# Performance work log

Hardware: AMD Instinct MI355X
Metric: run time of the kernel (lower is better)

The kernel has to match this reference:

```python
import jax, jax.numpy as jnp
import numpy as np

N_UP, N_DOWN = 8, 8
N_ELEC = N_UP + N_DOWN
N_NUC = 4
D, K, F, H = 128, 64, 32, 45  # embedding, kernel, dist_feat, w-MLP hidden (log-spaced)
CUTOFF = 10.0
B = 2048


def _pairs(a, b):
    s, r = np.meshgrid(a, b, indexing='ij')
    return s.ravel(), r.ravel()


def _edges():
    up = np.arange(N_UP)
    dn = np.arange(N_UP, N_ELEC)
    su, ru = _pairs(up, up); m = su != ru; su, ru = su[m], ru[m]
    sd, rd = _pairs(dn, dn); m = sd != rd; sd, rd = sd[m], rd[m]
    same_s = np.concatenate([su, sd]); same_r = np.concatenate([ru, rd])
    a1s, a1r = _pairs(up, dn); a2s, a2r = _pairs(dn, up)
    anti_s = np.concatenate([a1s, a2s]); anti_r = np.concatenate([a1r, a2r])
    ne_s = np.repeat(np.arange(N_NUC), N_ELEC)
    ne_r = np.tile(np.arange(N_ELEC), N_NUC)
    return tuple(jnp.asarray(x, jnp.int32) for x in (same_s, same_r, anti_s, anti_r, ne_s, ne_r))


def setup_inputs() -> dict:
    key = jax.random.key(0)
    ks = jax.random.split(key, 10)
    rs = jax.random.normal(ks[0], (B, N_ELEC, 3)) * 2.0
    coords = jax.random.normal(ks[1], (N_NUC, 3)) * 2.0
    X_tab = jax.random.normal(ks[2], (1, D))
    Y_w = jax.random.normal(ks[3], (N_NUC, K)) / np.sqrt(N_NUC)
    wW1 = jax.random.normal(ks[4], (3, 3, F, H)) / np.sqrt(F)
    wb1 = jax.random.normal(ks[5], (3, 3, H)) * 0.1
    wW2 = jax.random.normal(ks[6], (3, 3, H, K)) / np.sqrt(H)
    h0_tab = jax.random.normal(ks[7], (2, 1, K))
    hW = jax.random.normal(ks[8], (2, 2, D, K)) / np.sqrt(D)
    gW = jax.random.normal(ks[9], (3, 3, K, D)) / np.sqrt(K)
    same_s, same_r, anti_s, anti_r, ne_s, ne_r = _edges()
    return dict(rs=rs, coords=coords, X_tab=X_tab, Y_w=Y_w, wW1=wW1, wb1=wb1,
                wW2=wW2, h0_tab=h0_tab, hW=hW, gW=gW,
                same_s=same_s, same_r=same_r, anti_s=anti_s, anti_r=anti_r,
                ne_s=ne_s, ne_r=ne_r)


def _dist_basis(d):
    # DistanceBasis with 'nocusp' envelope: env = d^2 exp(-d), gaussians at mus
    qs = jnp.linspace(0.0, 1.0, F)
    mus = CUTOFF * qs ** 2
    sigmas = (1.0 + CUTOFF * qs) / 7.0
    env = d ** 2 * jnp.exp(-d)
    return env[..., None] * jnp.exp(-((d[..., None] - mus) ** 2) / sigmas ** 2)


def reference(rs, coords, X_tab, Y_w, wW1, wb1, wW2, h0_tab, hW, gW,
              same_s, same_r, anti_s, anti_r, ne_s, ne_r):
    Bn = rs.shape[0]
    spin_idxs = jnp.zeros((N_ELEC,), jnp.int32)  # n_up == n_down -> one spin class
    # per-edge distances (layer-0 update_edges_fn featurizes them once)
    d_same = jnp.linalg.norm(rs[:, same_s] - rs[:, same_r], axis=-1)  # [B,112]
    d_anti = jnp.linalg.norm(rs[:, anti_s] - rs[:, anti_r], axis=-1)  # [B,128]
    d_ne = jnp.linalg.norm(coords[ne_s][None] - rs[:, ne_r], axis=-1)  # [B,64]
    feats = [_dist_basis(d_same), _dist_basis(d_anti), _dist_basis(d_ne)]
    senders = [same_s, anti_s, ne_s]
    receivers = [same_r, anti_r, ne_r]
    elec = X_tab[spin_idxs]  # [N_ELEC, D] electron embedding X(spin_idxs)
    nuc = Y_w                # Y(eye(n_nuc)) == Y_w, [N_NUC, K]
    for l in range(3):
        upd = 0.0
        for j in range(3):  # same, anti, ne
            # w subnet: 2-layer MLP, silu hidden with bias, bias-free linear out
            we = jax.nn.silu(feats[j] @ wW1[l, j] + wb1[l, j]) @ wW2[l, j]  # [B,E,K]
            if j < 2:
                if l == 0:
                    hx = h0_tab[j][spin_idxs][senders[j]]            # [E,K] embed
                else:
                    hx = (elec @ hW[l - 1, j])[:, senders[j]]        # [B,E,K]
                weh = we * hx
            else:
                weh = we * nuc[ne_s][None]                           # [B,E,K]
            # segment_sum scatter into receiver electrons
            z = jnp.zeros((Bn, N_ELEC, K), we.dtype).at[:, receivers[j]].add(weh)
            upd = upd + z @ gW[l, j]                                  # [B,N_ELEC,D]
        elec = elec + upd
    return elec
```

## Files before the change

kernel.cpp:

```cpp
#include <hip/hip_runtime.h>
#include <hip/hip_bf16.h>

#define NE 16
#define NN 4
#define DDIM 128
#define KD 64
#define HD 45

typedef _Float16 half8 __attribute__((ext_vector_type(8)));
typedef _Float16 half4 __attribute__((ext_vector_type(4)));
typedef float floatx4 __attribute__((ext_vector_type(4)));

#define OFF_FLAG_B 0
#define OFF_B1_B   64
#define OFF_XT_B   1792
#define OFF_H0_B   2304
#define OFF_YW_B   2560
#define OFF_W1_B   3072
#define OFF_W2_B   30720
#define OFF_GW_B   104448
#define OFF_HW_B   251904
#define OFF_IND_B  317440

__device__ __forceinline__ float ldf(const void* p, long i, int f32) {
    if (f32) return ((const float*)p)[i];
    unsigned int u = ((unsigned int)((const unsigned short*)p)[i]) << 16;
    return __uint_as_float(u);
}

__global__ void prep2_kernel(const void* w1, const void* b1, const void* w2, const void* h0,
                             const void* hW, const void* gW, const void* Yw, const void* Xt,
                             const void* rs,
                             const int* __restrict__ same_r, const int* __restrict__ anti_r,
                             const int* __restrict__ ne_r, char* wsB) {
    __shared__ int badS;
    if (threadIdx.x == 0) badS = 0;
    __syncthreads();
    {
        const unsigned short* rs16 = (const unsigned short*)rs;
        int bad = 0;
        for (int i = threadIdx.x; i < 2048; i += 256) {
            unsigned int u = ((unsigned int)rs16[i]) << 16;
            float v = __uint_as_float(u);
            if (!(fabsf(v) < 1e6f)) bad = 1;
        }
        if (bad) atomicOr(&badS, 1);
    }
    __syncthreads();
    const int f32 = badS ? 1 : 0;
    if (blockIdx.x == 0 && threadIdx.x == 0) *(int*)(wsB + OFF_FLAG_B) = f32;

    int i = blockIdx.x * 256 + threadIdx.x;
    _Float16* W1F = (_Float16*)(wsB + OFF_W1_B);
    _Float16* W2F = (_Float16*)(wsB + OFF_W2_B);
    _Float16* GWF = (_Float16*)(wsB + OFF_GW_B);
    _Float16* HWF = (_Float16*)(wsB + OFF_HW_B);
    _Float16* INDF= (_Float16*)(wsB + OFF_IND_B);
    float*    B1  = (float*)(wsB + OFF_B1_B);
    float*    XT  = (float*)(wsB + OFF_XT_B);
    _Float16* H0F = (_Float16*)(wsB + OFF_H0_B);
    _Float16* YWF = (_Float16*)(wsB + OFF_YW_B);

    if (i < 13824) {
        int lj = i / 1536, rem = i % 1536;
        int nt = rem >> 9, lane = (rem & 511) >> 3, e = rem & 7;
        int row = ((lane >> 4) << 3) + e;
        int col = (nt << 4) + (lane & 15);
        W1F[i] = (_Float16)((col < 45) ? ldf(w1, lj * 1440 + row * 45 + col, f32) : 0.f);
    }
    if (i < 36864) {
        int lj = i / 4096, rem = i & 4095;
        int nt = rem >> 10, kt = (rem >> 9) & 1, lane = (rem & 511) >> 3, e = rem & 7;
        int row = (kt << 5) + ((lane >> 4) << 3) + e;
        int col = (nt << 4) + (lane & 15);
        W2F[i] = (_Float16)((row < 45) ? ldf(w2, lj * 2880 + row * 64 + col, f32) : 0.f);
    }
    if (i < 73728) {
        int lj = i >> 13, rem = i & 8191;
        int nt = rem >> 10, kt = (rem >> 9) & 1, lane = (rem & 511) >> 3, e = rem & 7;
        int row = (kt << 5) + ((lane >> 4) << 3) + e;
        int col = (nt << 4) + (lane & 15);
        GWF[i] = (_Float16)ldf(gW, lj * 8192 + row * 128 + col, f32);
    }
    if (i < 32768) {
        int lj = i >> 13, rem = i & 8191;
        int nt = rem >> 11, kt = (rem >> 9) & 3, lane = (rem & 511) >> 3, e = rem & 7;
        int row = (kt << 5) + ((lane >> 4) << 3) + e;
        int col = (nt << 4) + (lane & 15);
        HWF[i] = (_Float16)ldf(hW, lj * 8192 + row * 64 + col, f32);
    }
    if (i < 5120) {
        int c = i >> 9, rem = i & 511;
        int ln = rem >> 3, ii = rem & 7;
        int cls = (c < 4) ? 0 : ((c < 8) ? 1 : 2);
        int lc  = c - ((cls == 0) ? 0 : ((cls == 1) ? 4 : 8));
        int qd = ln >> 4, lm = ln & 15;
        int e = lc * 32 + qd * 8 + ii;
        int cnt = (cls == 0) ? 112 : ((cls == 1) ? 128 : 64);
        int r = 255;
        if (e < cnt) r = (cls == 0) ? same_r[e] : ((cls == 1) ? anti_r[e] : ne_r[e]);
        INDF[i] = (r == lm) ? (_Float16)1.0f : (_Float16)0.0f;
    }
    if (i < 432) { int lj = i / 48, n = i % 48; B1[i] = (n < 45) ? ldf(b1, lj * 45 + n, f32) : 0.f; }
    if (i < 128) XT[i] = ldf(Xt, i, f32);
    if (i < 128) H0F[i] = (_Float16)ldf(h0, i, f32);
    if (i < 256) YWF[i] = (_Float16)ldf(Yw, i, f32);
}

__device__ __forceinline__ half8 feat_tile(
    const void* __restrict__ rs, const void* __restrict__ coords,
    int b, int lm, int f32, int tloc, int cls,
    const int* __restrict__ S, const int* __restrict__ R,
    const float* __restrict__ A0, const float* __restrict__ B0, const float* __restrict__ C0)
{
    int le = tloc * 16 + lm;
    int s = S[le], r = R[le];
    long rb = ((long)b * NE + r) * 3;
    float bx = ldf(rs, rb + 0, f32), by = ldf(rs, rb + 1, f32), bz = ldf(rs, rb + 2, f32);
    float ax, ay, az;
    if (cls < 2) {
        long sb = ((long)b * NE + s) * 3;
        ax = ldf(rs, sb + 0, f32); ay = ldf(rs, sb + 1, f32); az = ldf(rs, sb + 2, f32);
    } else {
        ax = ldf(coords, s * 3 + 0, f32); ay = ldf(coords, s * 3 + 1, f32); az = ldf(coords, s * 3 + 2, f32);
    }
    float dx = ax - bx, dy = ay - by, dz = az - bz;
    float d = sqrtf(dx * dx + dy * dy + dz * dz);
    float d2 = d * d;
    half8 a;
    #pragma unroll
    for (int ii = 0; ii < 8; ++ii) {
        float E = fmaf(A0[ii], d2, fmaf(B0[ii], d, C0[ii]));
        a[ii] = (_Float16)(d2 * __expf(E));
    }
    return a;
}

__device__ __forceinline__ void we_tile_weh(
    half8 fa, int lj, int tile,
    const char* __restrict__ wsB, _Float16* __restrict__ hid,
    const _Float16* __restrict__ hxrow,
    const unsigned char* __restrict__ sendC,
    _Float16* __restrict__ wehT,
    int lane, int qd, int lm)
{
    const half8* W1F_lj = (const half8*)(wsB + OFF_W1_B) + lj * 192;
    half8 w0 = W1F_lj[lane], w1v = W1F_lj[64 + lane], w2v = W1F_lj[128 + lane];
    const float* B1 = (const float*)(wsB + OFF_B1_B) + lj * 48;
    float bi0 = B1[lm], bi1 = B1[16 + lm], bi2 = B1[32 + lm];
    floatx4 c0 = {0.f,0.f,0.f,0.f}, c1 = c0, c2 = c0;
    c0 = __builtin_amdgcn_mfma_f32_16x16x32_f16(fa, w0,  c0, 0, 0, 0);
    c1 = __builtin_amdgcn_mfma_f32_16x16x32_f16(fa, w1v, c1, 0, 0, 0);
    c2 = __builtin_amdgcn_mfma_f32_16x16x32_f16(fa, w2v, c2, 0, 0, 0);
    #pragma unroll
    for (int rr = 0; rr < 4; ++rr) {
        int row = qd * 4 + rr;
        int x = (row & 7) << 4;
        float v0 = c0[rr] + bi0, v1 = c1[rr] + bi1, v2 = c2[rr] + bi2;
        v0 = v0 * __builtin_amdgcn_rcpf(1.f + __expf(-v0));
        v1 = v1 * __builtin_amdgcn_rcpf(1.f + __expf(-v1));
        v2 = v2 * __builtin_amdgcn_rcpf(1.f + __expf(-v2));
        char* hb = (char*)hid + row * 128;
        *(_Float16*)(hb + ((lm * 2)      ^ x)) = (_Float16)v0;
        *(_Float16*)(hb + ((32 + lm * 2) ^ x)) = (_Float16)v1;
        *(_Float16*)(hb + ((64 + lm * 2) ^ x)) = (_Float16)v2;
    }
    int xr = (lm & 7) << 4;
    half8 a0 = *(const half8*)((const char*)hid + lm * 128 + ((qd * 16)      ^ xr));
    half8 a1 = *(const half8*)((const char*)hid + lm * 128 + ((64 + qd * 16) ^ xr));

    int sv0 = sendC[tile * 16 + qd * 4 + 0];
    int sv1 = sendC[tile * 16 + qd * 4 + 1];
    int sv2 = sendC[tile * 16 + qd * 4 + 2];
    int sv3 = sendC[tile * 16 + qd * 4 + 3];

    const half8* W2F_lj = (const half8*)(wsB + OFF_W2_B) + lj * 512;
    #pragma unroll
    for (int nt = 0; nt < 4; ++nt) {
        half8 bk0 = W2F_lj[nt * 128 + lane], bk1 = W2F_lj[nt * 128 + 64 + lane];
        floatx4 acc = {0.f,0.f,0.f,0.f};
        acc = __builtin_amdgcn_mfma_f32_16x16x32_f16(a0, bk0, acc, 0, 0, 0);
        acc = __builtin_amdgcn_mfma_f32_16x16x32_f16(a1, bk1, acc, 0, 0, 0);
        const int kc = nt * 16 + lm;
        const int eb = tile * 16 + qd * 4;
        wehT[kc * 136 + eb + 0] = (_Float16)(acc[0] * (float)hxrow[sv0 * 68 + kc]);
        wehT[kc * 136 + eb + 1] = (_Float16)(acc[1] * (float)hxrow[sv1 * 68 + kc]);
        wehT[kc * 136 + eb + 2] = (_Float16)(acc[2] * (float)hxrow[sv2 * 68 + kc]);
        wehT[kc * 136 + eb + 3] = (_Float16)(acc[3] * (float)hxrow[sv3 * 68 + kc]);
    }
}

__device__ __forceinline__ void z_mfma4(
    const _Float16* __restrict__ wehT, const half8* __restrict__ INDF, int c0,
    _Float16* __restrict__ zh, int wv, int qd, int lm, int lane)
{
    const _Float16* base = wehT + (wv * 16 + lm) * 136 + qd * 8;
    floatx4 zD = {0.f,0.f,0.f,0.f};
    zD = __builtin_amdgcn_mfma_f32_16x16x32_f16(*(const half8*)(base +  0), INDF[(c0 + 0) * 64 + lane], zD, 0, 0, 0);
    zD = __builtin_amdgcn_mfma_f32_16x16x32_f16(*(const half8*)(base + 32), INDF[(c0 + 1) * 64 + lane], zD, 0, 0, 0);
    zD = __builtin_amdgcn_mfma_f32_16x16x32_f16(*(const half8*)(base + 64), INDF[(c0 + 2) * 64 + lane], zD, 0, 0, 0);
    zD = __builtin_amdgcn_mfma_f32_16x16x32_f16(*(const half8*)(base + 96), INDF[(c0 + 3) * 64 + lane], zD, 0, 0, 0);
    half4 h;
    #pragma unroll
    for (int i = 0; i < 4; ++i) h[i] = (_Float16)zD[i];
    *(half4*)(zh + lm * 72 + wv * 16 + qd * 4) = h;
}

__device__ __forceinline__ void z_mfma2(
    const _Float16* __restrict__ wehT, const half8* __restrict__ INDF, int c0,
    _Float16* __restrict__ zh, int wv, int qd, int lm, int lane)
{
    const _Float16* base = wehT + (wv * 16 + lm) * 136 + qd * 8;
    floatx4 zD = {0.f,0.f,0.f,0.f};
    zD = __builtin_amdgcn_mfma_f32_16x16x32_f16(*(const half8*)(base +  0), INDF[(c0 + 0) * 64 + lane], zD, 0, 0, 0);
    zD = __builtin_amdgcn_mfma_f32_16x16x32_f16(*(const half8*)(base + 32), INDF[(c0 + 1) * 64 + lane], zD, 0, 0, 0);
    half4 h;
    #pragma unroll
    for (int i = 0; i < 4; ++i) h[i] = (_Float16)zD[i];
    *(half4*)(zh + lm * 72 + wv * 16 + qd * 4) = h;
}

__device__ __forceinline__ void gw_accum(
    int L, int j, int wv, int lane, int qd, int lm,
    const _Float16* __restrict__ zh, const half8* __restrict__ GWF, floatx4 (&eacc)[2])
{
    half8 zf0 = *(const half8*)(zh + lm * 72 + qd * 8);
    half8 zf1 = *(const half8*)(zh + lm * 72 + 32 + qd * 8);
    const half8* G = GWF + (size_t)(L * 3 + j) * 1024;
    #pragma unroll
    for (int u = 0; u < 2; ++u) {
        int t2 = wv * 2 + u;
        eacc[u] = __builtin_amdgcn_mfma_f32_16x16x32_f16(zf0, G[t2 * 128 + lane],      eacc[u], 0, 0, 0);
        eacc[u] = __builtin_amdgcn_mfma_f32_16x16x32_f16(zf1, G[t2 * 128 + 64 + lane], eacc[u], 0, 0, 0);
    }
}

__global__ __launch_bounds__(256, 2)
void fused_kernel(const void* __restrict__ rs, const void* __restrict__ coords,
                  const int* __restrict__ same_s, const int* __restrict__ same_r,
                  const int* __restrict__ anti_s, const int* __restrict__ anti_r,
                  const int* __restrict__ ne_s,   const int* __restrict__ ne_r,
                  const char* __restrict__ wsB, void* __restrict__ out)
{
    const int b = blockIdx.x;
    const int tid = threadIdx.x;
    const int wv = tid >> 6, lane = tid & 63;
    const int qd = lane >> 4, lm = lane & 15;
    const int f32 = *(const int*)(wsB + OFF_FLAG_B);

    __shared__ __align__(16) _Float16 wehT[64 * 136];
    __shared__ __align__(16) _Float16 hidA[4][1024];
    __shared__ __align__(16) _Float16 zhS[16 * 72];
    __shared__ _Float16 hxS[2 * 1088];
    __shared__ _Float16 nucS[4 * 68];
    __shared__ __align__(16) _Float16 elecB[16 * 136];
    __shared__ unsigned char sendPad[384];

    const _Float16* H0F = (const _Float16*)(wsB + OFF_H0_B);
    const _Float16* YWF = (const _Float16*)(wsB + OFF_YW_B);
    const float*    XT  = (const float*)(wsB + OFF_XT_B);
    const half8*    GWF = (const half8*)(wsB + OFF_GW_B);
    const half8*    HWF = (const half8*)(wsB + OFF_HW_B);
    const half8*    INDF= (const half8*)(wsB + OFF_IND_B);

    for (int i = tid; i < 384; i += 256) {
        int cls = i >> 7, pos = i & 127;
        int cnt = (cls == 0) ? 112 : ((cls == 1) ? 128 : 64);
        int s = 0;
        if (pos < cnt) {
            if (cls == 0)      s = same_s[pos];
            else if (cls == 1) s = anti_s[pos];
            else               s = ne_s[pos];
        }
        sendPad[i] = (unsigned char)s;
    }
    for (int i = tid; i < 2048; i += 256)
        hxS[(i >> 10) * 1088 + ((i >> 6) & 15) * 68 + (i & 63)] = H0F[((i >> 10) << 6) + (i & 63)];
    if (tid < 256) nucS[(tid >> 6) * 68 + (tid & 63)] = YWF[tid];
    for (int i = tid; i < 4352; i += 256) ((unsigned int*)wehT)[i] = 0u;
    {
        _Float16* hid = hidA[wv];
        half8 z8 = {0,0,0,0,0,0,0,0};
        *(half8*)(hid + lane * 8) = z8;
        *(half8*)(hid + 512 + lane * 8) = z8;
    }
    __syncthreads();

    half8 fa_s0, fa_s1 = {0,0,0,0,0,0,0,0}, fa_a0, fa_a1, fa_n;
    {
        float A0[8], B0[8], C0[8];
        #pragma unroll
        for (int ii = 0; ii < 8; ++ii) {
            float qf = (float)(qd * 8 + ii) * (1.f / 31.f);
            float mu = 10.f * qf * qf;
            float u = 7.f * __builtin_amdgcn_rcpf(1.f + 10.f * qf);
            float is2 = u * u;
            A0[ii] = -is2;
            B0[ii] = 2.f * mu * is2 - 1.f;
            C0[ii] = -(mu * mu) * is2;
        }
        fa_s0 = feat_tile(rs, coords, b, lm, f32, wv,     0, same_s, same_r, A0, B0, C0);
        if (wv < 3)
        fa_s1 = feat_tile(rs, coords, b, lm, f32, wv + 4, 0, same_s, same_r, A0, B0, C0);
        fa_a0 = feat_tile(rs, coords, b, lm, f32, wv,     1, anti_s, anti_r, A0, B0, C0);
        fa_a1 = feat_tile(rs, coords, b, lm, f32, wv + 4, 1, anti_s, anti_r, A0, B0, C0);
        fa_n  = feat_tile(rs, coords, b, lm, f32, wv,     2, ne_s,   ne_r,   A0, B0, C0);
    }

    floatx4 eacc[2];
    #pragma unroll
    for (int u = 0; u < 2; ++u) {
        float xv = XT[(wv * 2 + u) * 16 + lm];
        eacc[u][0] = xv; eacc[u][1] = xv; eacc[u][2] = xv; eacc[u][3] = xv;
    }

    _Float16* hid = hidA[wv];

    for (int L = 0; L < 3; ++L) {
        const int lj0 = L * 3;
        we_tile_weh(fa_s0, lj0, wv, wsB, hid, hxS, sendPad, wehT, lane, qd, lm);
        if (wv < 3)
        we_tile_weh(fa_s1, lj0, wv + 4, wsB, hid, hxS, sendPad, wehT, lane, qd, lm);
        __syncthreads();
        z_mfma4(wehT, INDF, 0, zhS, wv, qd, lm, lane);
        __syncthreads();
        gw_accum(L, 0, wv, lane, qd, lm, zhS, GWF, eacc);
        we_tile_weh(fa_a0, lj0 + 1, wv,     wsB, hid, hxS + 1088, sendPad + 128, wehT, lane, qd, lm);
        we_tile_weh(fa_a1, lj0 + 1, wv + 4, wsB, hid, hxS + 1088, sendPad + 128, wehT, lane, qd, lm);
        __syncthreads();
        z_mfma4(wehT, INDF, 4, zhS, wv, qd, lm, lane);
        __syncthreads();
        gw_accum(L, 1, wv, lane, qd, lm, zhS, GWF, eacc);
        we_tile_weh(fa_n, lj0 + 2, wv, wsB, hid, nucS, sendPad + 256, wehT, lane, qd, lm);
        __syncthreads();
        z_mfma2(wehT, INDF, 8, zhS, wv, qd, lm, lane);
        __syncthreads();
        gw_accum(L, 2, wv, lane, qd, lm, zhS, GWF, eacc);

        if (L < 2) {
            #pragma unroll
            for (int u = 0; u < 2; ++u) {
                int t2 = wv * 2 + u;
                #pragma unroll
                for (int r = 0; r < 4; ++r)
                    elecB[(qd * 4 + r) * 136 + t2 * 16 + lm] = (_Float16)eacc[u][r];
            }
            __syncthreads();
            half8 ae[4];
            #pragma unroll
            for (int kt = 0; kt < 4; ++kt)
                ae[kt] = *(const half8*)(elecB + lm * 136 + kt * 32 + qd * 8);
            #pragma unroll
            for (int u = 0; u < 2; ++u) {
                int idx = wv * 2 + u;
                int j = idx >> 2, nt = idx & 3;
                floatx4 acc = {0.f,0.f,0.f,0.f};
                #pragma unroll
                for (int kt = 0; kt < 4; ++kt) {
                    half8 g = HWF[(size_t)(((L * 2 + j) * 4 + nt) * 4 + kt) * 64 + lane];
                    acc = __builtin_amdgcn_mfma_f32_16x16x32_f16(ae[kt], g, acc, 0, 0, 0);
                }
                #pragma unroll
                for (int r = 0; r < 4; ++r)
                    hxS[j * 1088 + (qd * 4 + r) * 68 + nt * 16 + lm] = (_Float16)acc[r];
            }
            __syncthreads();
        }
    }

    if (f32) {
        float* o = (float*)out + (size_t)b * 2048;
        #pragma unroll
        for (int u = 0; u < 2; ++u)
            #pragma unroll
            for (int r = 0; r < 4; ++r)
                o[(qd * 4 + r) * 128 + (wv * 2 + u) * 16 + lm] = eacc[u][r];
    } else {
        __hip_bfloat16* o = (__hip_bfloat16*)out + (size_t)b * 2048;
        #pragma unroll
        for (int u = 0; u < 2; ++u)
            #pragma unroll
            for (int r = 0; r < 4; ++r)
                o[(qd * 4 + r) * 128 + (wv * 2 + u) * 16 + lm] = __float2bfloat16(eacc[u][r]);
    }
}

extern "C" void kernel_launch(void* const* d_in, const int* in_sizes, int n_in,
                              void* d_out, int out_size, void* d_ws, size_t ws_size,
                              hipStream_t stream) {
    const void* rs     = d_in[0];
    const void* coords = d_in[1];
    const void* X_tab  = d_in[2];
    const void* Y_w    = d_in[3];
    const void* wW1    = d_in[4];
    const void* wb1    = d_in[5];
    const void* wW2    = d_in[6];
    const void* h0     = d_in[7];
    const void* hW     = d_in[8];
    const void* gW     = d_in[9];
    const int* same_s = (const int*)d_in[10];
    const int* same_r = (const int*)d_in[11];
    const int* anti_s = (const int*)d_in[12];
    const int* anti_r = (const int*)d_in[13];
    const int* ne_s   = (const int*)d_in[14];
    const int* ne_r   = (const int*)d_in[15];
    char* wsB = (char*)d_ws;

    const int Bn = in_sizes[0] / (NE * 3);

    prep2_kernel<<<288, 256, 0, stream>>>(wW1, wb1, wW2, h0, hW, gW, Y_w, X_tab, rs,
                                          same_r, anti_r, ne_r, wsB);
    fused_kernel<<<Bn, 256, 0, stream>>>(rs, coords, same_s, same_r, anti_s, anti_r,
                                         ne_s, ne_r, wsB, d_out);
}
```

Baseline: 187.0 us.

## Process two batch samples per block to amortize barriers and weight loads

Each workgroup now handles two batch elements, duplicating the LDS scratch buffers and interleaving both samples' stages between the same barriers. Each barrier and each block's setup now covers twice the work, and the two independent chains give the scheduler more instructions to overlap. The per-block weh writes also become packed half4 stores instead of scalar stores. In exchange, LDS use roughly doubles and register pressure rises, which can lower occupancy, and the grid is halved to 1024 blocks.

```diff
diff --git a/kernel.cpp b/kernel.cpp
--- a/kernel.cpp
+++ b/kernel.cpp
@@ -183,10 +183,12 @@
         acc = __builtin_amdgcn_mfma_f32_16x16x32_f16(a1, bk1, acc, 0, 0, 0);
         const int kc = nt * 16 + lm;
         const int eb = tile * 16 + qd * 4;
-        wehT[kc * 136 + eb + 0] = (_Float16)(acc[0] * (float)hxrow[sv0 * 68 + kc]);
-        wehT[kc * 136 + eb + 1] = (_Float16)(acc[1] * (float)hxrow[sv1 * 68 + kc]);
-        wehT[kc * 136 + eb + 2] = (_Float16)(acc[2] * (float)hxrow[sv2 * 68 + kc]);
-        wehT[kc * 136 + eb + 3] = (_Float16)(acc[3] * (float)hxrow[sv3 * 68 + kc]);
+        half4 hv;
+        hv[0] = (_Float16)(acc[0] * (float)hxrow[sv0 * 68 + kc]);
+        hv[1] = (_Float16)(acc[1] * (float)hxrow[sv1 * 68 + kc]);
+        hv[2] = (_Float16)(acc[2] * (float)hxrow[sv2 * 68 + kc]);
+        hv[3] = (_Float16)(acc[3] * (float)hxrow[sv3 * 68 + kc]);
+        *(half4*)(wehT + kc * 136 + eb) = hv;
     }
 }
 
@@ -235,25 +237,52 @@
     }
 }
 
+__device__ __forceinline__ void hx_update(
+    int L, int wv, int lane, int qd, int lm,
+    const _Float16* __restrict__ elecB, const half8* __restrict__ HWF,
+    _Float16* __restrict__ hxS)
+{
+    half8 ae0 = *(const half8*)(elecB + lm * 136 +  0 + qd * 8);
+    half8 ae1 = *(const half8*)(elecB + lm * 136 + 32 + qd * 8);
+    half8 ae2 = *(const half8*)(elecB + lm * 136 + 64 + qd * 8);
+    half8 ae3 = *(const half8*)(elecB + lm * 136 + 96 + qd * 8);
+    #pragma unroll
+    for (int u = 0; u < 2; ++u) {
+        int idx = wv * 2 + u;
+        int j = idx >> 2, nt = idx & 3;
+        const half8* Bb = HWF + (size_t)(((L * 2 + j) * 4 + nt) * 4) * 64;
+        floatx4 acc = {0.f,0.f,0.f,0.f};
+        acc = __builtin_amdgcn_mfma_f32_16x16x32_f16(ae0, Bb[  0 + lane], acc, 0, 0, 0);
+        acc = __builtin_amdgcn_mfma_f32_16x16x32_f16(ae1, Bb[ 64 + lane], acc, 0, 0, 0);
+        acc = __builtin_amdgcn_mfma_f32_16x16x32_f16(ae2, Bb[128 + lane], acc, 0, 0, 0);
+        acc = __builtin_amdgcn_mfma_f32_16x16x32_f16(ae3, Bb[192 + lane], acc, 0, 0, 0);
+        #pragma unroll
+        for (int r = 0; r < 4; ++r)
+            hxS[j * 1088 + (qd * 4 + r) * 68 + nt * 16 + lm] = (_Float16)acc[r];
+    }
+}
+
 __global__ __launch_bounds__(256, 2)
 void fused_kernel(const void* __restrict__ rs, const void* __restrict__ coords,
                   const int* __restrict__ same_s, const int* __restrict__ same_r,
                   const int* __restrict__ anti_s, const int* __restrict__ anti_r,
                   const int* __restrict__ ne_s,   const int* __restrict__ ne_r,
-                  const char* __restrict__ wsB, void* __restrict__ out)
-{
-    const int b = blockIdx.x;
+                  const char* __restrict__ wsB, void* __restrict__ out, int Bn)
+{
+    const int b0 = blockIdx.x * 2;
+    const int b1 = b0 + 1;
+    const bool has1 = (b1 < Bn);
     const int tid = threadIdx.x;
     const int wv = tid >> 6, lane = tid & 63;
     const int qd = lane >> 4, lm = lane & 15;
     const int f32 = *(const int*)(wsB + OFF_FLAG_B);
 
-    __shared__ __align__(16) _Float16 wehT[64 * 136];
-    __shared__ __align__(16) _Float16 hidA[4][1024];
-    __shared__ __align__(16) _Float16 zhS[16 * 72];
-    __shared__ _Float16 hxS[2 * 1088];
+    __shared__ __align__(16) _Float16 wehT0[64 * 136], wehT1[64 * 136];
+    __shared__ __align__(16) _Float16 hid0A[4][1024], hid1A[4][1024];
+    __shared__ __align__(16) _Float16 zh0S[16 * 72], zh1S[16 * 72];
+    __shared__ _Float16 hx0S[2 * 1088], hx1S[2 * 1088];
     __shared__ _Float16 nucS[4 * 68];
-    __shared__ __align__(16) _Float16 elecB[16 * 136];
+    __shared__ __align__(16) _Float16 elec0B[16 * 136], elec1B[16 * 136];
     __shared__ unsigned char sendPad[384];
 
     const _Float16* H0F = (const _Float16*)(wsB + OFF_H0_B);
@@ -274,19 +303,27 @@
         }
         sendPad[i] = (unsigned char)s;
     }
-    for (int i = tid; i < 2048; i += 256)
-        hxS[(i >> 10) * 1088 + ((i >> 6) & 15) * 68 + (i & 63)] = H0F[((i >> 10) << 6) + (i & 63)];
+    for (int i = tid; i < 2048; i += 256) {
+        _Float16 v = H0F[((i >> 10) << 6) + (i & 63)];
+        int off = (i >> 10) * 1088 + ((i >> 6) & 15) * 68 + (i & 63);
+        hx0S[off] = v; hx1S[off] = v;
+    }
     if (tid < 256) nucS[(tid >> 6) * 68 + (tid & 63)] = YWF[tid];
-    for (int i = tid; i < 4352; i += 256) ((unsigned int*)wehT)[i] = 0u;
+    for (int i = tid; i < 4352; i += 256) {
+        ((unsigned int*)wehT0)[i] = 0u; ((unsigned int*)wehT1)[i] = 0u;
+    }
     {
-        _Float16* hid = hidA[wv];
         half8 z8 = {0,0,0,0,0,0,0,0};
-        *(half8*)(hid + lane * 8) = z8;
-        *(half8*)(hid + 512 + lane * 8) = z8;
+        *(half8*)(hid0A[wv] + lane * 8) = z8;
+        *(half8*)(hid0A[wv] + 512 + lane * 8) = z8;
+        *(half8*)(hid1A[wv] + lane * 8) = z8;
+        *(half8*)(hid1A[wv] + 512 + lane * 8) = z8;
     }
     __syncthreads();
 
-    half8 fa_s0, fa_s1 = {0,0,0,0,0,0,0,0}, fa_a0, fa_a1, fa_n;
+    half8 fs0_0, fs1_0 = {0,0,0,0,0,0,0,0}, fa0_0, fa1_0, fn_0;
+    half8 fs0_1 = {0,0,0,0,0,0,0,0}, fs1_1 = {0,0,0,0,0,0,0,0};
+    half8 fa0_1 = {0,0,0,0,0,0,0,0}, fa1_1 = {0,0,0,0,0,0,0,0}, fn_1 = {0,0,0,0,0,0,0,0};
     {
         float A0[8], B0[8], C0[8];
         #pragma unroll
@@ -299,89 +336,118 @@
             B0[ii] = 2.f * mu * is2 - 1.f;
             C0[ii] = -(mu * mu) * is2;
         }
-        fa_s0 = feat_tile(rs, coords, b, lm, f32, wv,     0, same_s, same_r, A0, B0, C0);
+        fs0_0 = feat_tile(rs, coords, b0, lm, f32, wv,     0, same_s, same_r, A0, B0, C0);
         if (wv < 3)
-        fa_s1 = feat_tile(rs, coords, b, lm, f32, wv + 4, 0, same_s, same_r, A0, B0, C0);
-        fa_a0 = feat_tile(rs, coords, b, lm, f32, wv,     1, anti_s, anti_r, A0, B0, C0);
-        fa_a1 = feat_tile(rs, coords, b, lm, f32, wv + 4, 1, anti_s, anti_r, A0, B0, C0);
-        fa_n  = feat_tile(rs, coords, b, lm, f32, wv,     2, ne_s,   ne_r,   A0, B0, C0);
-    }
-
-    floatx4 eacc[2];
+        fs1_0 = feat_tile(rs, coords, b0, lm, f32, wv + 4, 0, same_s, same_r, A0, B0, C0);
+        fa0_0 = feat_tile(rs, coords, b0, lm, f32, wv,     1, anti_s, anti_r, A0, B0, C0);
+        fa1_0 = feat_tile(rs, coords, b0, lm, f32, wv + 4, 1, anti_s, anti_r, A0, B0, C0);
+        fn_0  = feat_tile(rs, coords, b0, lm, f32, wv,     2, ne_s,   ne_r,   A0, B0, C0);
+        if (has1) {
+            fs0_1 = feat_tile(rs, coords, b1, lm, f32, wv,     0, same_s, same_r, A0, B0, C0);
+            if (wv < 3)
+            fs1_1 = feat_tile(rs, coords, b1, lm, f32, wv + 4, 0, same_s, same_r, A0, B0, C0);
+            fa0_1 = feat_tile(rs, coords, b1, lm, f32, wv,     1, anti_s, anti_r, A0, B0, C0);
+            fa1_1 = feat_tile(rs, coords, b1, lm, f32, wv + 4, 1, anti_s, anti_r, A0, B0, C0);
+            fn_1  = feat_tile(rs, coords, b1, lm, f32, wv,     2, ne_s,   ne_r,   A0, B0, C0);
+        }
+    }
+
+    floatx4 eacc0[2], eacc1[2];
     #pragma unroll
     for (int u = 0; u < 2; ++u) {
         float xv = XT[(wv * 2 + u) * 16 + lm];
-        eacc[u][0] = xv; eacc[u][1] = xv; eacc[u][2] = xv; eacc[u][3] = xv;
-    }
-
-    _Float16* hid = hidA[wv];
+        eacc0[u][0] = xv; eacc0[u][1] = xv; eacc0[u][2] = xv; eacc0[u][3] = xv;
+        eacc1[u] = eacc0[u];
+    }
+
+    _Float16* hid0 = hid0A[wv];
+    _Float16* hid1 = hid1A[wv];
 
     for (int L = 0; L < 3; ++L) {
         const int lj0 = L * 3;
-        we_tile_weh(fa_s0, lj0, wv, wsB, hid, hxS, sendPad, wehT, lane, qd, lm);
+        we_tile_weh(fs0_0, lj0, wv, wsB, hid0, hx0S, sendPad, wehT0, lane, qd, lm);
         if (wv < 3)
-        we_tile_weh(fa_s1, lj0, wv + 4, wsB, hid, hxS, sendPad, wehT, lane, qd, lm);
-        __syncthreads();
-        z_mfma4(wehT, INDF, 0, zhS, wv, qd, lm, lane);
-        __syncthreads();
-        gw_accum(L, 0, wv, lane, qd, lm, zhS, GWF, eacc);
-        we_tile_weh(fa_a0, lj0 + 1, wv,     wsB, hid, hxS + 1088, sendPad + 128, wehT, lane, qd, lm);
-        we_tile_weh(fa_a1, lj0 + 1, wv + 4, wsB, hid, hxS + 1088, sendPad + 128, wehT, lane, qd, lm);
-        __syncthreads();
-        z_mfma4(wehT, INDF, 4, zhS, wv, qd, lm, lane);
-        __syncthreads();
-        gw_accum(L, 1, wv, lane, qd, lm, zhS, GWF, eacc);
-        we_tile_weh(fa_n, lj0 + 2, wv, wsB, hid, nucS, sendPad + 256, wehT, lane, qd, lm);
-        __syncthreads();
-        z_mfma2(wehT, INDF, 8, zhS, wv, qd, lm, lane);
-        __syncthreads();
-        gw_accum(L, 2, wv, lane, qd, lm, zhS, GWF, eacc);
+        we_tile_weh(fs1_0, lj0, wv + 4, wsB, hid0, hx0S, sendPad, wehT0, lane, qd, lm);
+        if (has1) {
+            we_tile_weh(fs0_1, lj0, wv, wsB, hid1, hx1S, sendPad, wehT1, lane, qd, lm);
+            if (wv < 3)
+            we_tile_weh(fs1_1, lj0, wv + 4, wsB, hid1, hx1S, sendPad, wehT1, lane, qd, lm);
+        }
+        __syncthreads();
+        z_mfma4(wehT0, INDF, 0, zh0S, wv, qd, lm, lane);
+        if (has1) z_mfma4(wehT1, INDF, 0, zh1S, wv, qd, lm, lane);
+        __syncthreads();
+        gw_accum(L, 0, wv, lane, qd, lm, zh0S, GWF, eacc0);
+        if (has1) gw_accum(L, 0, wv, lane, qd, lm, zh1S, GWF, eacc1);
+        we_tile_weh(fa0_0, lj0 + 1, wv,     wsB, hid0, hx0S + 1088, sendPad + 128, wehT0, lane, qd, lm);
+        we_tile_weh(fa1_0, lj0 + 1, wv + 4, wsB, hid0, hx0S + 1088, sendPad + 128, wehT0, lane, qd, lm);
+        if (has1) {
+            we_tile_weh(fa0_1, lj0 + 1, wv,     wsB, hid1, hx1S + 1088, sendPad + 128, wehT1, lane, qd, lm);
+            we_tile_weh(fa1_1, lj0 + 1, wv + 4, wsB, hid1, hx1S + 1088, sendPad + 128, wehT1, lane, qd, lm);
+        }
+        __syncthreads();
+        z_mfma4(wehT0, INDF, 4, zh0S, wv, qd, lm, lane);
+        if (has1) z_mfma4(wehT1, INDF, 4, zh1S, wv, qd, lm, lane);
+        __syncthreads();
+        gw_accum(L, 1, wv, lane, qd, lm, zh0S, GWF, eacc0);
+        if (has1) gw_accum(L, 1, wv, lane, qd, lm, zh1S, GWF, eacc1);
+        we_tile_weh(fn_0, lj0 + 2, wv, wsB, hid0, nucS, sendPad + 256, wehT0, lane, qd, lm);
+        if (has1)
+        we_tile_weh(fn_1, lj0 + 2, wv, wsB, hid1, nucS, sendPad + 256, wehT1, lane, qd, lm);
+        __syncthreads();
+        z_mfma2(wehT0, INDF, 8, zh0S, wv, qd, lm, lane);
+        if (has1) z_mfma2(wehT1, INDF, 8, zh1S, wv, qd, lm, lane);
+        __syncthreads();
+        gw_accum(L, 2, wv, lane, qd, lm, zh0S, GWF, eacc0);
+        if (has1) gw_accum(L, 2, wv, lane, qd, lm, zh1S, GWF, eacc1);
 
         if (L < 2) {
             #pragma unroll
             for (int u = 0; u < 2; ++u) {
                 int t2 = wv * 2 + u;
                 #pragma unroll
-                for (int r = 0; r < 4; ++r)
-                    elecB[(qd * 4 + r) * 136 + t2 * 16 + lm] = (_Float16)eacc[u][r];
+                for (int r = 0; r < 4; ++r) {
+                    elec0B[(qd * 4 + r) * 136 + t2 * 16 + lm] = (_Float16)eacc0[u][r];
+                    elec1B[(qd * 4 + r) * 136 + t2 * 16 + lm] = (_Float16)eacc1[u][r];
+                }
             }
             __syncthreads();
-            half8 ae[4];
-            #pragma unroll
-            for (int kt = 0; kt < 4; ++kt)
-                ae[kt] = *(const half8*)(elecB + lm * 136 + kt * 32 + qd * 8);
-            #pragma unroll
-            for (int u = 0; u < 2; ++u) {
-                int idx = wv * 2 + u;
-                int j = idx >> 2, nt = idx & 3;
-                floatx4 acc = {0.f,0.f,0.f,0.f};
-                #pragma unroll
-                for (int kt = 0; kt < 4; ++kt) {
-                    half8 g = HWF[(size_t)(((L * 2 + j) * 4 + nt) * 4 + kt) * 64 + lane];
-                    acc = __builtin_amdgcn_mfma_f32_16x16x32_f16(ae[kt], g, acc, 0, 0, 0);
-                }
-                #pragma unroll
-                for (int r = 0; r < 4; ++r)
-                    hxS[j * 1088 + (qd * 4 + r) * 68 + nt * 16 + lm] = (_Float16)acc[r];
-            }
+            hx_update(L, wv, lane, qd, lm, elec0B, HWF, hx0S);
+            if (has1) hx_update(L, wv, lane, qd, lm, elec1B, HWF, hx1S);
             __syncthreads();
         }
     }
 
     if (f32) {
-        float* o = (float*)out + (size_t)b * 2048;
+        float* o0 = (float*)out + (size_t)b0 * 2048;
         #pragma unroll
         for (int u = 0; u < 2; ++u)
             #pragma unroll
             for (int r = 0; r < 4; ++r)
-                o[(qd * 4 + r) * 128 + (wv * 2 + u) * 16 + lm] = eacc[u][r];
+                o0[(qd * 4 + r) * 128 + (wv * 2 + u) * 16 + lm] = eacc0[u][r];
+        if (has1) {
+            float* o1 = (float*)out + (size_t)b1 * 2048;
+            #pragma unroll
+            for (int u = 0; u < 2; ++u)
+                #pragma unroll
+                for (int r = 0; r < 4; ++r)
+                    o1[(qd * 4 + r) * 128 + (wv * 2 + u) * 16 + lm] = eacc1[u][r];
+        }
     } else {
-        __hip_bfloat16* o = (__hip_bfloat16*)out + (size_t)b * 2048;
+        __hip_bfloat16* o0 = (__hip_bfloat16*)out + (size_t)b0 * 2048;
         #pragma unroll
         for (int u = 0; u < 2; ++u)
             #pragma unroll
             for (int r = 0; r < 4; ++r)
-                o[(qd * 4 + r) * 128 + (wv * 2 + u) * 16 + lm] = __float2bfloat16(eacc[u][r]);
+                o0[(qd * 4 + r) * 128 + (wv * 2 + u) * 16 + lm] = __float2bfloat16(eacc0[u][r]);
+        if (has1) {
+            __hip_bfloat16* o1 = (__hip_bfloat16*)out + (size_t)b1 * 2048;
+            #pragma unroll
+            for (int u = 0; u < 2; ++u)
+                #pragma unroll
+                for (int r = 0; r < 4; ++r)
+                    o1[(qd * 4 + r) * 128 + (wv * 2 + u) * 16 + lm] = __float2bfloat16(eacc1[u][r]);
+        }
     }
 }
 
@@ -410,6 +476,7 @@
 
     prep2_kernel<<<288, 256, 0, stream>>>(wW1, wb1, wW2, h0, hW, gW, Y_w, X_tab, rs,
                                           same_r, anti_r, ne_r, wsB);
-    fused_kernel<<<Bn, 256, 0, stream>>>(rs, coords, same_s, same_r, anti_s, anti_r,
-                                         ne_s, ne_r, wsB, d_out);
-}
+    fused_kernel<<<(Bn + 1) / 2, 256, 0, stream>>>(rs, coords, same_s, same_r,
+                                                   anti_s, anti_r, ne_s, ne_r,
+                                                   wsB, d_out, Bn);
+}
```

After: 200.3 us. 7.1% more time.

## Batch all three edge types per layer to cut block barriers

Applied to the files above, without the earlier changes.

Each layer now computes the we*hx products for the same, anti and nuclear edge types into one wider wehT buffer, using distinct column offsets. The scatter MFMAs for all three types then run in one phase, and the gW accumulation runs over six K-chunks. This drops the per-layer __syncthreads count from six to two and gives each wave more independent MFMA work between barriers. The cost is larger LDS buffers (wehT stride 328, zhS stride 200), which may limit occupancy. The wehT stores are also packed into half4 writes.

```diff
diff --git a/kernel.cpp b/kernel.cpp
--- a/kernel.cpp
+++ b/kernel.cpp
@@ -21,6 +21,8 @@
 #define OFF_GW_B   104448
 #define OFF_HW_B   251904
 #define OFF_IND_B  317440
+
+#define WSTRIDE 328
 
 __device__ __forceinline__ float ldf(const void* p, long i, int f32) {
     if (f32) return ((const float*)p)[i];
@@ -137,7 +139,7 @@
 }
 
 __device__ __forceinline__ void we_tile_weh(
-    half8 fa, int lj, int tile,
+    half8 fa, int lj, int tloc, int cbase,
     const char* __restrict__ wsB, _Float16* __restrict__ hid,
     const _Float16* __restrict__ hxrow,
     const unsigned char* __restrict__ sendC,
@@ -169,12 +171,13 @@
     half8 a0 = *(const half8*)((const char*)hid + lm * 128 + ((qd * 16)      ^ xr));
     half8 a1 = *(const half8*)((const char*)hid + lm * 128 + ((64 + qd * 16) ^ xr));
 
-    int sv0 = sendC[tile * 16 + qd * 4 + 0];
-    int sv1 = sendC[tile * 16 + qd * 4 + 1];
-    int sv2 = sendC[tile * 16 + qd * 4 + 2];
-    int sv3 = sendC[tile * 16 + qd * 4 + 3];
+    int sv0 = sendC[tloc * 16 + qd * 4 + 0];
+    int sv1 = sendC[tloc * 16 + qd * 4 + 1];
+    int sv2 = sendC[tloc * 16 + qd * 4 + 2];
+    int sv3 = sendC[tloc * 16 + qd * 4 + 3];
 
     const half8* W2F_lj = (const half8*)(wsB + OFF_W2_B) + lj * 512;
+    const int eb = cbase + tloc * 16 + qd * 4;
     #pragma unroll
     for (int nt = 0; nt < 4; ++nt) {
         half8 bk0 = W2F_lj[nt * 128 + lane], bk1 = W2F_lj[nt * 128 + 64 + lane];
@@ -182,56 +185,37 @@
         acc = __builtin_amdgcn_mfma_f32_16x16x32_f16(a0, bk0, acc, 0, 0, 0);
         acc = __builtin_amdgcn_mfma_f32_16x16x32_f16(a1, bk1, acc, 0, 0, 0);
         const int kc = nt * 16 + lm;
-        const int eb = tile * 16 + qd * 4;
-        wehT[kc * 136 + eb + 0] = (_Float16)(acc[0] * (float)hxrow[sv0 * 68 + kc]);
-        wehT[kc * 136 + eb + 1] = (_Float16)(acc[1] * (float)hxrow[sv1 * 68 + kc]);
-        wehT[kc * 136 + eb + 2] = (_Float16)(acc[2] * (float)hxrow[sv2 * 68 + kc]);
-        wehT[kc * 136 + eb + 3] = (_Float16)(acc[3] * (float)hxrow[sv3 * 68 + kc]);
-    }
-}
-
-__device__ __forceinline__ void z_mfma4(
-    const _Float16* __restrict__ wehT, const half8* __restrict__ INDF, int c0,
-    _Float16* __restrict__ zh, int wv, int qd, int lm, int lane)
+        half4 hv;
+        hv[0] = (_Float16)(acc[0] * (float)hxrow[sv0 * 68 + kc]);
+        hv[1] = (_Float16)(acc[1] * (float)hxrow[sv1 * 68 + kc]);
+        hv[2] = (_Float16)(acc[2] * (float)hxrow[sv2 * 68 + kc]);
+        hv[3] = (_Float16)(acc[3] * (float)hxrow[sv3 * 68 + kc]);
+        *(half4*)(wehT + kc * WSTRIDE + eb) = hv;
+    }
+}
+
+__device__ __forceinline__ void hx_update(
+    int L, int wv, int lane, int qd, int lm,
+    const _Float16* __restrict__ elecB, const half8* __restrict__ HWF,
+    _Float16* __restrict__ hxS)
 {
-    const _Float16* base = wehT + (wv * 16 + lm) * 136 + qd * 8;
-    floatx4 zD = {0.f,0.f,0.f,0.f};
-    zD = __builtin_amdgcn_mfma_f32_16x16x32_f16(*(const half8*)(base +  0), INDF[(c0 + 0) * 64 + lane], zD, 0, 0, 0);
-    zD = __builtin_amdgcn_mfma_f32_16x16x32_f16(*(const half8*)(base + 32), INDF[(c0 + 1) * 64 + lane], zD, 0, 0, 0);
-    zD = __builtin_amdgcn_mfma_f32_16x16x32_f16(*(const half8*)(base + 64), INDF[(c0 + 2) * 64 + lane], zD, 0, 0, 0);
-    zD = __builtin_amdgcn_mfma_f32_16x16x32_f16(*(const half8*)(base + 96), INDF[(c0 + 3) * 64 + lane], zD, 0, 0, 0);
-    half4 h;
-    #pragma unroll
-    for (int i = 0; i < 4; ++i) h[i] = (_Float16)zD[i];
-    *(half4*)(zh + lm * 72 + wv * 16 + qd * 4) = h;
-}
-
-__device__ __forceinline__ void z_mfma2(
-    const _Float16* __restrict__ wehT, const half8* __restrict__ INDF, int c0,
-    _Float16* __restrict__ zh, int wv, int qd, int lm, int lane)
-{
-    const _Float16* base = wehT + (wv * 16 + lm) * 136 + qd * 8;
-    floatx4 zD = {0.f,0.f,0.f,0.f};
-    zD = __builtin_amdgcn_mfma_f32_16x16x32_f16(*(const half8*)(base +  0), INDF[(c0 + 0) * 64 + lane], zD, 0, 0, 0);
-    zD = __builtin_amdgcn_mfma_f32_16x16x32_f16(*(const half8*)(base + 32), INDF[(c0 + 1) * 64 + lane], zD, 0, 0, 0);
-    half4 h;
-    #pragma unroll
-    for (int i = 0; i < 4; ++i) h[i] = (_Float16)zD[i];
-    *(half4*)(zh + lm * 72 + wv * 16 + qd * 4) = h;
-}
-
-__device__ __forceinline__ void gw_accum(
-    int L, int j, int wv, int lane, int qd, int lm,
-    const _Float16* __restrict__ zh, const half8* __restrict__ GWF, floatx4 (&eacc)[2])
-{
-    half8 zf0 = *(const half8*)(zh + lm * 72 + qd * 8);
-    half8 zf1 = *(const half8*)(zh + lm * 72 + 32 + qd * 8);
-    const half8* G = GWF + (size_t)(L * 3 + j) * 1024;
+    half8 ae0 = *(const half8*)(elecB + lm * 136 +  0 + qd * 8);
+    half8 ae1 = *(const half8*)(elecB + lm * 136 + 32 + qd * 8);
+    half8 ae2 = *(const half8*)(elecB + lm * 136 + 64 + qd * 8);
+    half8 ae3 = *(const half8*)(elecB + lm * 136 + 96 + qd * 8);
     #pragma unroll
     for (int u = 0; u < 2; ++u) {
-        int t2 = wv * 2 + u;
-        eacc[u] = __builtin_amdgcn_mfma_f32_16x16x32_f16(zf0, G[t2 * 128 + lane],      eacc[u], 0, 0, 0);
-        eacc[u] = __builtin_amdgcn_mfma_f32_16x16x32_f16(zf1, G[t2 * 128 + 64 + lane], eacc[u], 0, 0, 0);
+        int idx = wv * 2 + u;
+        int j = idx >> 2, nt = idx & 3;
+        const half8* Bb = HWF + (size_t)(((L * 2 + j) * 4 + nt) * 4) * 64;
+        floatx4 acc = {0.f,0.f,0.f,0.f};
+        acc = __builtin_amdgcn_mfma_f32_16x16x32_f16(ae0, Bb[  0 + lane], acc, 0, 0, 0);
+        acc = __builtin_amdgcn_mfma_f32_16x16x32_f16(ae1, Bb[ 64 + lane], acc, 0, 0, 0);
+        acc = __builtin_amdgcn_mfma_f32_16x16x32_f16(ae2, Bb[128 + lane], acc, 0, 0, 0);
+        acc = __builtin_amdgcn_mfma_f32_16x16x32_f16(ae3, Bb[192 + lane], acc, 0, 0, 0);
+        #pragma unroll
+        for (int r = 0; r < 4; ++r)
+            hxS[j * 1088 + (qd * 4 + r) * 68 + nt * 16 + lm] = (_Float16)acc[r];
     }
 }
 
@@ -248,9 +232,9 @@
     const int qd = lane >> 4, lm = lane & 15;
     const int f32 = *(const int*)(wsB + OFF_FLAG_B);
 
-    __shared__ __align__(16) _Float16 wehT[64 * 136];
+    __shared__ __align__(16) _Float16 wehT[64 * WSTRIDE];
     __shared__ __align__(16) _Float16 hidA[4][1024];
-    __shared__ __align__(16) _Float16 zhS[16 * 72];
+    __shared__ __align__(16) _Float16 zhS[16 * 200];
     __shared__ _Float16 hxS[2 * 1088];
     __shared__ _Float16 nucS[4 * 68];
     __shared__ __align__(16) _Float16 elecB[16 * 136];
@@ -277,7 +261,7 @@
     for (int i = tid; i < 2048; i += 256)
         hxS[(i >> 10) * 1088 + ((i >> 6) & 15) * 68 + (i & 63)] = H0F[((i >> 10) << 6) + (i & 63)];
     if (tid < 256) nucS[(tid >> 6) * 68 + (tid & 63)] = YWF[tid];
-    for (int i = tid; i < 4352; i += 256) ((unsigned int*)wehT)[i] = 0u;
+    for (int i = tid; i < 64 * WSTRIDE / 2; i += 256) ((unsigned int*)wehT)[i] = 0u;
     {
         _Float16* hid = hidA[wv];
         half8 z8 = {0,0,0,0,0,0,0,0};
@@ -318,24 +302,51 @@
 
     for (int L = 0; L < 3; ++L) {
         const int lj0 = L * 3;
-        we_tile_weh(fa_s0, lj0, wv, wsB, hid, hxS, sendPad, wehT, lane, qd, lm);
+        we_tile_weh(fa_s0, lj0,     wv,     0,   wsB, hid, hxS,        sendPad,       wehT, lane, qd, lm);
         if (wv < 3)
-        we_tile_weh(fa_s1, lj0, wv + 4, wsB, hid, hxS, sendPad, wehT, lane, qd, lm);
+        we_tile_weh(fa_s1, lj0,     wv + 4, 0,   wsB, hid, hxS,        sendPad,       wehT, lane, qd, lm);
+        we_tile_weh(fa_a0, lj0 + 1, wv,     128, wsB, hid, hxS + 1088, sendPad + 128, wehT, lane, qd, lm);
+        we_tile_weh(fa_a1, lj0 + 1, wv + 4, 128, wsB, hid, hxS + 1088, sendPad + 128, wehT, lane, qd, lm);
+        we_tile_weh(fa_n,  lj0 + 2, wv,     256, wsB, hid, nucS,       sendPad + 256, wehT, lane, qd, lm);
         __syncthreads();
-        z_mfma4(wehT, INDF, 0, zhS, wv, qd, lm, lane);
+
+        {
+            const _Float16* baseA = wehT + (wv * 16 + lm) * WSTRIDE + qd * 8;
+            floatx4 z0 = {0.f,0.f,0.f,0.f};
+            z0 = __builtin_amdgcn_mfma_f32_16x16x32_f16(*(const half8*)(baseA +   0), INDF[0 * 64 + lane], z0, 0, 0, 0);
+            z0 = __builtin_amdgcn_mfma_f32_16x16x32_f16(*(const half8*)(baseA +  32), INDF[1 * 64 + lane], z0, 0, 0, 0);
+            z0 = __builtin_amdgcn_mfma_f32_16x16x32_f16(*(const half8*)(baseA +  64), INDF[2 * 64 + lane], z0, 0, 0, 0);
+            z0 = __builtin_amdgcn_mfma_f32_16x16x32_f16(*(const half8*)(baseA +  96), INDF[3 * 64 + lane], z0, 0, 0, 0);
+            floatx4 z1 = {0.f,0.f,0.f,0.f};
+            z1 = __builtin_amdgcn_mfma_f32_16x16x32_f16(*(const half8*)(baseA + 128), INDF[4 * 64 + lane], z1, 0, 0, 0);
+            z1 = __builtin_amdgcn_mfma_f32_16x16x32_f16(*(const half8*)(baseA + 160), INDF[5 * 64 + lane], z1, 0, 0, 0);
+            z1 = __builtin_amdgcn_mfma_f32_16x16x32_f16(*(const half8*)(baseA + 192), INDF[6 * 64 + lane], z1, 0, 0, 0);
+            z1 = __builtin_amdgcn_mfma_f32_16x16x32_f16(*(const half8*)(baseA + 224), INDF[7 * 64 + lane], z1, 0, 0, 0);
+            floatx4 z2 = {0.f,0.f,0.f,0.f};
+            z2 = __builtin_amdgcn_mfma_f32_16x16x32_f16(*(const half8*)(baseA + 256), INDF[8 * 64 + lane], z2, 0, 0, 0);
+            z2 = __builtin_amdgcn_mfma_f32_16x16x32_f16(*(const half8*)(baseA + 288), INDF[9 * 64 + lane], z2, 0, 0, 0);
+            half4 h0v, h1v, h2v;
+            #pragma unroll
+            for (int i = 0; i < 4; ++i) {
+                h0v[i] = (_Float16)z0[i]; h1v[i] = (_Float16)z1[i]; h2v[i] = (_Float16)z2[i];
+            }
+            _Float16* zr = zhS + lm * 200 + wv * 16 + qd * 4;
+            *(half4*)(zr +   0) = h0v;
+            *(half4*)(zr +  64) = h1v;
+            *(half4*)(zr + 128) = h2v;
+        }
         __syncthreads();
-        gw_accum(L, 0, wv, lane, qd, lm, zhS, GWF, eacc);
-        we_tile_weh(fa_a0, lj0 + 1, wv,     wsB, hid, hxS + 1088, sendPad + 128, wehT, lane, qd, lm);
-        we_tile_weh(fa_a1, lj0 + 1, wv + 4, wsB, hid, hxS + 1088, sendPad + 128, wehT, lane, qd, lm);
-        __syncthreads();
-        z_mfma4(wehT, INDF, 4, zhS, wv, qd, lm, lane);
-        __syncthreads();
-        gw_accum(L, 1, wv, lane, qd, lm, zhS, GWF, eacc);
-        we_tile_weh(fa_n, lj0 + 2, wv, wsB, hid, nucS, sendPad + 256, wehT, lane, qd, lm);
-        __syncthreads();
-        z_mfma2(wehT, INDF, 8, zhS, wv, qd, lm, lane);
-        __syncthreads();
-        gw_accum(L, 2, wv, lane, qd, lm, zhS, GWF, eacc);
+
+        #pragma unroll
+        for (int u = 0; u < 2; ++u) {
+            int t2 = wv * 2 + u;
+            #pragma unroll
+            for (int c = 0; c < 6; ++c) {
+                half8 zf = *(const half8*)(zhS + lm * 200 + c * 32 + qd * 8);
+                const half8* G = GWF + (size_t)(lj0 + (c >> 1)) * 1024;
+                eacc[u] = __builtin_amdgcn_mfma_f32_16x16x32_f16(zf, G[t2 * 128 + (c & 1) * 64 + lane], eacc[u], 0, 0, 0);
+            }
+        }
 
         if (L < 2) {
             #pragma unroll
@@ -346,24 +357,7 @@
                     elecB[(qd * 4 + r) * 136 + t2 * 16 + lm] = (_Float16)eacc[u][r];
             }
             __syncthreads();
-            half8 ae[4];
-            #pragma unroll
-            for (int kt = 0; kt < 4; ++kt)
-                ae[kt] = *(const half8*)(elecB + lm * 136 + kt * 32 + qd * 8);
-            #pragma unroll
-            for (int u = 0; u < 2; ++u) {
-                int idx = wv * 2 + u;
-                int j = idx >> 2, nt = idx & 3;
-                floatx4 acc = {0.f,0.f,0.f,0.f};
-                #pragma unroll
-                for (int kt = 0; kt < 4; ++kt) {
-                    half8 g = HWF[(size_t)(((L * 2 + j) * 4 + nt) * 4 + kt) * 64 + lane];
-                    acc = __builtin_amdgcn_mfma_f32_16x16x32_f16(ae[kt], g, acc, 0, 0, 0);
-                }
-                #pragma unroll
-                for (int r = 0; r < 4; ++r)
-                    hxS[j * 1088 + (qd * 4 + r) * 68 + nt * 16 + lm] = (_Float16)acc[r];
-            }
+            hx_update(L, wv, lane, qd, lm, elecB, HWF, hxS);
             __syncthreads();
         }
     }
```

Result: no change. 188.7 us (+0.9%).
